# Optimization experiments

Hardware: AMD Instinct MI355X
Metric: run time of the kernel (lower is better)

The kernel has to match this reference:

```python
import jax, jax.numpy as jnp
import numpy as np

H = 1024      # hidden_dim
NH = 16       # num_heads
HD = H // NH  # head_dim
FFN = 4096
EPS = 1e-5


def setup_inputs() -> dict:
    key = jax.random.key(0)
    ks = jax.random.split(key, 12)
    s = 0.02
    return {
        "x": jax.random.normal(ks[0], (2, 2048, H), dtype=jnp.float32),
        "w_qkv": jax.random.normal(ks[1], (H, 3 * H), dtype=jnp.float32) * s,
        "b_qkv": jnp.zeros((3 * H,), dtype=jnp.float32),
        "w_out": jax.random.normal(ks[2], (H, H), dtype=jnp.float32) * s,
        "b_out": jnp.zeros((H,), dtype=jnp.float32),
        "ln1_g": jnp.ones((H,), dtype=jnp.float32),
        "ln1_b": jnp.zeros((H,), dtype=jnp.float32),
        "ln2_g": jnp.ones((H,), dtype=jnp.float32),
        "ln2_b": jnp.zeros((H,), dtype=jnp.float32),
        "w1": jax.random.normal(ks[3], (H, FFN), dtype=jnp.float32) * s,
        "b1": jnp.zeros((FFN,), dtype=jnp.float32),
        "w2": jax.random.normal(ks[4], (FFN, H), dtype=jnp.float32) * s,
        "b2": jnp.zeros((H,), dtype=jnp.float32),
    }


def _layernorm(x, g, b):
    mu = jnp.mean(x, axis=-1, keepdims=True)
    var = jnp.mean(jnp.square(x - mu), axis=-1, keepdims=True)
    return (x - mu) * jax.lax.rsqrt(var + EPS) * g + b


def reference(x, w_qkv, b_qkv, w_out, b_out, ln1_g, ln1_b, ln2_g, ln2_b, w1, b1, w2, b2):
    B, S, _ = x.shape
    # pre-LN attention branch
    h = _layernorm(x, ln1_g, ln1_b)
    qkv = h @ w_qkv + b_qkv                       # (B,S,3H)
    qkv = qkv.reshape(B, S, 3, NH, HD).transpose(2, 0, 3, 1, 4)
    q, k, v = qkv[0], qkv[1], qkv[2]              # (B,NH,S,HD)
    scores = jnp.einsum("bhqd,bhkd->bhqk", q, k) / jnp.sqrt(jnp.float32(HD))
    causal = jnp.triu(jnp.ones((S, S), dtype=bool), k=1)
    scores = jnp.where(causal, -jnp.inf, scores)
    attn = jax.nn.softmax(scores, axis=-1)
    out = jnp.einsum("bhqk,bhkd->bhqd", attn, v)  # (B,NH,S,HD)
    out = out.transpose(0, 2, 1, 3).reshape(B, S, H)
    attn_out = out @ w_out + b_out
    x = x + attn_out
    # FFN branch
    h2 = _layernorm(x, ln2_g, ln2_b)
    ffn = jax.nn.gelu(h2 @ w1 + b1, approximate=False) @ w2 + b2
    return x + ffn
```

## Files before the change

kernel.cpp:

```cpp
#include <hip/hip_runtime.h>
#include <hip/hip_bf16.h>

typedef __bf16 bf16_t;
typedef __bf16 bf16x8 __attribute__((ext_vector_type(8)));
typedef __bf16 bf16x4 __attribute__((ext_vector_type(4)));
typedef __bf16 bf16x2 __attribute__((ext_vector_type(2)));
typedef float  f32x4  __attribute__((ext_vector_type(4)));

#define HDIM 1024
#define SEQ  2048
#define NHEAD 16
#define HEADD 64

__device__ __forceinline__ void gld_lds16(const void* g, void* l) {
  __builtin_amdgcn_global_load_lds(
      (const __attribute__((address_space(1))) unsigned int*)g,
      (__attribute__((address_space(3))) unsigned int*)l, 16, 0, 0);
}

__global__ __launch_bounds__(256) void ln_kernel(const float* __restrict__ x,
                                                 const float* __restrict__ gam,
                                                 const float* __restrict__ bet,
                                                 bf16_t* __restrict__ out) {
  int row = blockIdx.x;
  int t = threadIdx.x;
  const float4* xr = (const float4*)(x + (size_t)row * HDIM);
  float4 v = xr[t];
  float s = v.x + v.y + v.z + v.w;
  float ss = v.x*v.x + v.y*v.y + v.z*v.z + v.w*v.w;
  #pragma unroll
  for (int o = 32; o > 0; o >>= 1) {
    s  += __shfl_xor(s, o);
    ss += __shfl_xor(ss, o);
  }
  __shared__ float red[8];
  int w = t >> 6;
  if ((t & 63) == 0) { red[w*2] = s; red[w*2+1] = ss; }
  __syncthreads();
  s  = red[0] + red[2] + red[4] + red[6];
  ss = red[1] + red[3] + red[5] + red[7];
  float mu  = s * (1.0f / HDIM);
  float var = ss * (1.0f / HDIM) - mu * mu;
  float rstd = rsqrtf(var + 1e-5f);
  float4 g4 = ((const float4*)gam)[t];
  float4 b4 = ((const float4*)bet)[t];
  bf16x4 o4;
  o4[0] = (bf16_t)((v.x - mu) * rstd * g4.x + b4.x);
  o4[1] = (bf16_t)((v.y - mu) * rstd * g4.y + b4.y);
  o4[2] = (bf16_t)((v.z - mu) * rstd * g4.z + b4.z);
  o4[3] = (bf16_t)((v.w - mu) * rstd * g4.w + b4.w);
  *(bf16x4*)(out + (size_t)row * HDIM + t * 4) = o4;
}

__global__ __launch_bounds__(256) void transpose_cast(const float* __restrict__ W,
                                                      bf16_t* __restrict__ Wt,
                                                      int Kd, int Nd) {
  __shared__ float tile[32][33];
  int n0 = blockIdx.x * 32, k0 = blockIdx.y * 32;
  int tx = threadIdx.x & 31, ty = threadIdx.x >> 5;
  #pragma unroll
  for (int i = 0; i < 4; i++)
    tile[ty + i*8][tx] = W[(size_t)(k0 + ty + i*8) * Nd + n0 + tx];
  __syncthreads();
  #pragma unroll
  for (int i = 0; i < 4; i++)
    Wt[(size_t)(n0 + ty + i*8) * Kd + k0 + tx] = (bf16_t)tile[tx][ty + i*8];
}

__device__ __forceinline__ float gelu_fast(float x) {
  float y = 0.7978845608f * (x + 0.044715f * x * x * x);
  float u = exp2f(y * 2.885390082f);
  float th = 1.0f - 2.0f * __builtin_amdgcn_rcpf(u + 1.0f);
  return 0.5f * x * (1.0f + th);
}

template<int EPI, int BN>
__global__ __launch_bounds__(256, 2)
void gemm_bt(const bf16_t* __restrict__ A, const bf16_t* __restrict__ Bt,
             const float* __restrict__ bias, const float* __restrict__ resid,
             void* __restrict__ outp, int M, int N, int K) {
  constexpr int NFRAG = BN / 32;
  __shared__ bf16_t As[2][128*64];
  __shared__ bf16_t Bs[2][BN*64];
  int t = threadIdx.x;
  int w = t >> 6, l = t & 63;
  int wr = w >> 1, wc = w & 1;

  int nbx = gridDim.x;
  int bid = blockIdx.y * nbx + blockIdx.x;
  int chunkx = (nbx * gridDim.y) >> 3;
  int nb = (bid & 7) * chunkx + (bid >> 3);
  int bm = nb / nbx, bn = nb % nbx;
  size_t m0 = (size_t)bm * 128, n0 = (size_t)bn * BN;

  f32x4 acc[4][NFRAG];
  #pragma unroll
  for (int m = 0; m < 4; m++)
    #pragma unroll
    for (int n = 0; n < NFRAG; n++) acc[m][n] = (f32x4)(0.0f);

  int srow = t >> 3;
  int scol = ((t & 7) ^ (srow & 7)) * 8;
  int dsto = t * 8;
  const bf16_t* ag = A  + (m0 + srow) * K + scol;
  const bf16_t* bg = Bt + (n0 + srow) * K + scol;

  int lr = l & 15, lg = l >> 4;

  auto stage = [&](int buf, int k0) {
    #pragma unroll
    for (int p = 0; p < 4; p++)
      gld_lds16(ag + k0 + (size_t)(p*32)*K, &As[buf][dsto + p*32*64]);
    #pragma unroll
    for (int p = 0; p < BN/32; p++)
      gld_lds16(bg + k0 + (size_t)(p*32)*K, &Bs[buf][dsto + p*32*64]);
  };

  stage(0, 0);
  __syncthreads();
  int cur = 0;
  const int NK = K / 64;
  for (int k = 0; k < NK; k++) {
    if (k + 1 < NK) stage(cur ^ 1, (k + 1) * 64);
    #pragma unroll
    for (int kk = 0; kk < 2; kk++) {
      bf16x8 af[4], bfr[NFRAG];
      #pragma unroll
      for (int m = 0; m < 4; m++) {
        int row = wr*64 + m*16 + lr;
        int off = row*128 + (((kk*4 + lg) ^ (row & 7)) << 4);
        af[m] = *(const bf16x8*)((const char*)&As[cur][0] + off);
      }
      #pragma unroll
      for (int n = 0; n < NFRAG; n++) {
        int row = wc*(BN/2) + n*16 + lr;
        int off = row*128 + (((kk*4 + lg) ^ (row & 7)) << 4);
        bfr[n] = *(const bf16x8*)((const char*)&Bs[cur][0] + off);
      }
      #pragma unroll
      for (int m = 0; m < 4; m++)
        #pragma unroll
        for (int n = 0; n < NFRAG; n++)
          acc[m][n] = __builtin_amdgcn_mfma_f32_16x16x32_bf16(af[m], bfr[n], acc[m][n], 0, 0, 0);
    }
    __syncthreads();
    cur ^= 1;
  }

  int r0 = (l >> 4) * 4, c0 = l & 15;
  #pragma unroll
  for (int m = 0; m < 4; m++) {
    #pragma unroll
    for (int n = 0; n < NFRAG; n++) {
      size_t row = m0 + wr*64 + m*16 + r0;
      size_t col = n0 + wc*(BN/2) + n*16 + c0;
      float bv = bias[col];
      #pragma unroll
      for (int r = 0; r < 4; r++) {
        float vv = acc[m][n][r] + bv;
        size_t idx = (row + r) * (size_t)N + col;
        if (EPI == 0) {
          ((bf16_t*)outp)[idx] = (bf16_t)vv;
        } else if (EPI == 1) {
          ((float*)outp)[idx] = vv + resid[idx];
        } else {
          ((bf16_t*)outp)[idx] = (bf16_t)gelu_fast(vv);
        }
      }
    }
  }
}

__global__ __launch_bounds__(512, 4)
void attn_kernel(const bf16_t* __restrict__ qkv, bf16_t* __restrict__ out) {
  int idx = blockIdx.x;
  int half = idx >> 8;
  int sub = idx & 255;
  int qth = sub >> 5;
  int qt = half ? qth : (15 - qth);
  int bh = sub & 31;
  int b = bh >> 4, h = bh & 15;
  int t = threadIdx.x, w = t >> 6, l = t & 63;

  __shared__ bf16_t Ks[2][64*64];
  __shared__ bf16_t Vt[2][64*72];
  __shared__ bf16_t Ps[8][16*64];

  const size_t RS = 3 * HDIM;
  const bf16_t* qb = qkv + (size_t)b * SEQ * RS + h * HEADD;
  const bf16_t* kb = qb + HDIM;
  const bf16_t* vb = qb + 2 * HDIM;

  int lr = l & 15, lg = l >> 4;
  const float SCALE = 0.125f * 1.44269504f;

  bf16x8 qf[2];
  {
    size_t qrow = (size_t)qt * 128 + w * 16 + lr;
    qf[0] = *(const bf16x8*)(qb + qrow * RS + lg * 8);
    qf[1] = *(const bf16x8*)(qb + qrow * RS + 32 + lg * 8);
    #pragma unroll
    for (int i = 0; i < 8; i++) {
      qf[0][i] = (bf16_t)((float)qf[0][i] * SCALE);
      qf[1][i] = (bf16_t)((float)qf[1][i] * SCALE);
    }
  }

  f32x4 o[4];
  #pragma unroll
  for (int d = 0; d < 4; d++) o[d] = (f32x4)(0.0f);
  float m = -1e30f, lsum = 0.0f;

  int srow = t >> 3, scol = (t & 7) * 8;
  int Fv = ((scol >> 3) & 7) << 3;
  int nkt = 2 * qt + 2;

  const bf16_t* kg0 = kb + (size_t)srow * RS + scol;
  const bf16_t* vg0 = vb + (size_t)srow * RS + scol;

  bf16x8 kr = *(const bf16x8*)kg0;
  bf16x8 vr = *(const bf16x8*)vg0;

  int wrow0 = qt * 128 + w * 16;
  int qg = wrow0 + lr;
  bf16_t* pw = Ps[w];
  int psw = (lr & 7) << 4;
  int cur = 0;

  for (int kt = 0; kt < nkt; kt++) {
    {
      int ba = srow * 128 + scol * 2;
      int sw = (srow & 7) << 4;
      *(bf16x8*)((char*)Ks[cur] + (ba ^ sw)) = kr;
      int ksw = srow ^ Fv;
      bf16_t* vt = Vt[cur];
      #pragma unroll
      for (int i = 0; i < 8; i++)
        vt[(scol + i) * 72 + ksw] = vr[i];
    }
    if (kt + 1 < nkt) {
      kr = *(const bf16x8*)(kg0 + (size_t)(kt + 1) * 64 * RS);
      vr = *(const bf16x8*)(vg0 + (size_t)(kt + 1) * 64 * RS);
    }
    __syncthreads();

    bool skipw = (kt * 64) > (wrow0 + 15);
    if (!skipw) {
      f32x4 sc[4];
      #pragma unroll
      for (int kt2 = 0; kt2 < 4; kt2++) {
        sc[kt2] = (f32x4)(0.0f);
        #pragma unroll
        for (int kk = 0; kk < 2; kk++) {
          int row = kt2 * 16 + lr;
          int off = (row * 128 + kk * 64 + lg * 16) ^ ((row & 7) << 4);
          bf16x8 kf = *(const bf16x8*)((char*)Ks[cur] + off);
          sc[kt2] = __builtin_amdgcn_mfma_f32_16x16x32_bf16(kf, qf[kk], sc[kt2], 0, 0, 0);
        }
      }
      if (kt * 64 + 63 > wrow0) {
        #pragma unroll
        for (int kt2 = 0; kt2 < 4; kt2++) {
          #pragma unroll
          for (int r = 0; r < 4; r++) {
            int kcol = kt*64 + kt2*16 + lg*4 + r;
            if (kcol > qg) sc[kt2][r] = -1e30f;
          }
        }
      }
      float tm0 = fmaxf(fmaxf(sc[0][0], sc[0][1]), fmaxf(sc[0][2], sc[0][3]));
      float tm1 = fmaxf(fmaxf(sc[1][0], sc[1][1]), fmaxf(sc[1][2], sc[1][3]));
      float tm2 = fmaxf(fmaxf(sc[2][0], sc[2][1]), fmaxf(sc[2][2], sc[2][3]));
      float tm3 = fmaxf(fmaxf(sc[3][0], sc[3][1]), fmaxf(sc[3][2], sc[3][3]));
      float tm = fmaxf(fmaxf(tm0, tm1), fmaxf(tm2, tm3));
      tm = fmaxf(tm, __shfl_xor(tm, 16));
      tm = fmaxf(tm, __shfl_xor(tm, 32));
      if (!__all(tm <= m + 8.0f)) {
        float nm = fmaxf(m, tm);
        float alpha = exp2f(m - nm);
        m = nm;
        lsum *= alpha;
        #pragma unroll
        for (int d = 0; d < 4; d++)
          #pragma unroll
          for (int r = 0; r < 4; r++) o[d][r] *= alpha;
      }
      #pragma unroll
      for (int kt2 = 0; kt2 < 4; kt2++) {
        float p0 = exp2f(sc[kt2][0] - m);
        float p1 = exp2f(sc[kt2][1] - m);
        float p2 = exp2f(sc[kt2][2] - m);
        float p3 = exp2f(sc[kt2][3] - m);
        lsum += (p0 + p1) + (p2 + p3);
        bf16x2 pa; pa[0] = (bf16_t)p0; pa[1] = (bf16_t)p1;
        bf16x2 pb; pb[0] = (bf16_t)p2; pb[1] = (bf16_t)p3;
        int base = lr * 128 + kt2 * 32 + lg * 8;
        *(bf16x2*)((char*)pw + ((base)     ^ psw)) = pa;
        *(bf16x2*)((char*)pw + ((base + 4) ^ psw)) = pb;
      }
      asm volatile("s_waitcnt lgkmcnt(0)" ::: "memory");
      #pragma unroll
      for (int kk = 0; kk < 2; kk++) {
        int poff = (lr * 128 + kk * 64 + lg * 16) ^ psw;
        bf16x8 pf = *(const bf16x8*)((char*)pw + poff);
        #pragma unroll
        for (int dblk = 0; dblk < 4; dblk++) {
          int vrow = dblk * 16 + lr;
          int Fd = ((vrow >> 3) & 7) << 3;
          bf16x8 vf = *(const bf16x8*)(Vt[cur] + vrow * 72 + ((kk * 32 + lg * 8) ^ Fd));
          o[dblk] = __builtin_amdgcn_mfma_f32_16x16x32_bf16(vf, pf, o[dblk], 0, 0, 0);
        }
      }
    }
    cur ^= 1;
  }

  lsum += __shfl_xor(lsum, 16);
  lsum += __shfl_xor(lsum, 32);
  float inv = 1.0f / lsum;

  bf16_t* ob = out + ((size_t)b * SEQ + qg) * HDIM + h * HEADD;
  #pragma unroll
  for (int dblk = 0; dblk < 4; dblk++) {
    bf16x4 q4;
    #pragma unroll
    for (int r = 0; r < 4; r++) q4[r] = (bf16_t)(o[dblk][r] * inv);
    *(bf16x4*)(ob + dblk * 16 + lg * 4) = q4;
  }
}

extern "C" void kernel_launch(void* const* d_in, const int* in_sizes, int n_in,
                              void* d_out, int out_size, void* d_ws, size_t ws_size,
                              hipStream_t stream) {
  (void)in_sizes; (void)n_in; (void)out_size; (void)ws_size;
  const float* x     = (const float*)d_in[0];
  const float* w_qkv = (const float*)d_in[1];
  const float* b_qkv = (const float*)d_in[2];
  const float* w_out = (const float*)d_in[3];
  const float* b_out = (const float*)d_in[4];
  const float* ln1_g = (const float*)d_in[5];
  const float* ln1_b = (const float*)d_in[6];
  const float* ln2_g = (const float*)d_in[7];
  const float* ln2_b = (const float*)d_in[8];
  const float* w1    = (const float*)d_in[9];
  const float* b1    = (const float*)d_in[10];
  const float* w2    = (const float*)d_in[11];
  const float* b2    = (const float*)d_in[12];
  float* out = (float*)d_out;

  char* ws = (char*)d_ws;
  size_t off = 0;
  auto alloc = [&](size_t bytes) -> void* {
    void* p = ws + off;
    off += (bytes + 255) & ~(size_t)255;
    return p;
  };
  bf16_t* wqkvT = (bf16_t*)alloc((size_t)3072*1024*2);
  bf16_t* woutT = (bf16_t*)alloc((size_t)1024*1024*2);
  bf16_t* w1T   = (bf16_t*)alloc((size_t)4096*1024*2);
  bf16_t* w2T   = (bf16_t*)alloc((size_t)1024*4096*2);
  bf16_t* ln1o  = (bf16_t*)alloc((size_t)4096*1024*2);
  bf16_t* qkvb  = (bf16_t*)alloc((size_t)4096*4096*2);
  bf16_t* attno = (bf16_t*)alloc((size_t)4096*1024*2);
  float*  x2    = (float*) alloc((size_t)4096*1024*4);
  bf16_t* h2 = ln1o;
  bf16_t* g  = qkvb;

  dim3 blk(256);
  transpose_cast<<<dim3(3072/32, 1024/32), blk, 0, stream>>>(w_qkv, wqkvT, 1024, 3072);
  transpose_cast<<<dim3(1024/32, 1024/32), blk, 0, stream>>>(w_out, woutT, 1024, 1024);
  transpose_cast<<<dim3(4096/32, 1024/32), blk, 0, stream>>>(w1,    w1T,   1024, 4096);
  transpose_cast<<<dim3(1024/32, 4096/32), blk, 0, stream>>>(w2,    w2T,   4096, 1024);

  ln_kernel<<<4096, blk, 0, stream>>>(x, ln1_g, ln1_b, ln1o);
  gemm_bt<0,128><<<dim3(24, 32), blk, 0, stream>>>(ln1o, wqkvT, b_qkv, nullptr, qkvb, 4096, 3072, 1024);
  attn_kernel<<<512, dim3(512), 0, stream>>>(qkvb, attno);
  gemm_bt<1,64><<<dim3(16, 32), blk, 0, stream>>>(attno, woutT, b_out, x, x2, 4096, 1024, 1024);
  ln_kernel<<<4096, blk, 0, stream>>>(x2, ln2_g, ln2_b, h2);
  gemm_bt<2,128><<<dim3(32, 32), blk, 0, stream>>>(h2, w1T, b1, nullptr, g, 4096, 4096, 1024);
  gemm_bt<1,64><<<dim3(16, 32), blk, 0, stream>>>(g, w2T, b2, x2, out, 4096, 1024, 4096);
}
```

Before: 237.8 us.

## Split-K the FFN down-projection GEMM with a bf16 partial reduce kernel

Result: faster. 231.2 us (-2.8%).

```diff
diff --git a/kernel.cpp b/kernel.cpp
--- a/kernel.cpp
+++ b/kernel.cpp
@@ -74,7 +74,32 @@
   return 0.5f * x * (1.0f + th);
 }
 
-template<int EPI, int BN>
+__global__ __launch_bounds__(256)
+void reduce2_kernel(const bf16_t* __restrict__ p0, const bf16_t* __restrict__ p1,
+                    const float* __restrict__ bias, const float* __restrict__ resid,
+                    float* __restrict__ out) {
+  size_t base = ((size_t)blockIdx.x * 256 + threadIdx.x) * 8;
+  bf16x8 a = *(const bf16x8*)(p0 + base);
+  bf16x8 b = *(const bf16x8*)(p1 + base);
+  int col = (int)(base & (HDIM - 1));
+  float4 bi0 = *(const float4*)(bias + col);
+  float4 bi1 = *(const float4*)(bias + col + 4);
+  float4 r0 = *(const float4*)(resid + base);
+  float4 r1 = *(const float4*)(resid + base + 4);
+  float4 o0, o1;
+  o0.x = (float)a[0] + (float)b[0] + bi0.x + r0.x;
+  o0.y = (float)a[1] + (float)b[1] + bi0.y + r0.y;
+  o0.z = (float)a[2] + (float)b[2] + bi0.z + r0.z;
+  o0.w = (float)a[3] + (float)b[3] + bi0.w + r0.w;
+  o1.x = (float)a[4] + (float)b[4] + bi1.x + r1.x;
+  o1.y = (float)a[5] + (float)b[5] + bi1.y + r1.y;
+  o1.z = (float)a[6] + (float)b[6] + bi1.z + r1.z;
+  o1.w = (float)a[7] + (float)b[7] + bi1.w + r1.w;
+  *(float4*)(out + base)     = o0;
+  *(float4*)(out + base + 4) = o1;
+}
+
+template<int EPI, int BN, int SPLITK>
 __global__ __launch_bounds__(256, 2)
 void gemm_bt(const bf16_t* __restrict__ A, const bf16_t* __restrict__ Bt,
              const float* __restrict__ bias, const float* __restrict__ resid,
@@ -93,6 +118,9 @@
   int bm = nb / nbx, bn = nb % nbx;
   size_t m0 = (size_t)bm * 128, n0 = (size_t)bn * BN;
 
+  const int KK = (SPLITK > 1) ? K / SPLITK : K;
+  const size_t koff = (SPLITK > 1) ? (size_t)blockIdx.z * KK : 0;
+
   f32x4 acc[4][NFRAG];
   #pragma unroll
   for (int m = 0; m < 4; m++)
@@ -102,8 +130,8 @@
   int srow = t >> 3;
   int scol = ((t & 7) ^ (srow & 7)) * 8;
   int dsto = t * 8;
-  const bf16_t* ag = A  + (m0 + srow) * K + scol;
-  const bf16_t* bg = Bt + (n0 + srow) * K + scol;
+  const bf16_t* ag = A  + (m0 + srow) * K + koff + scol;
+  const bf16_t* bg = Bt + (n0 + srow) * K + koff + scol;
 
   int lr = l & 15, lg = l >> 4;
 
@@ -119,7 +147,7 @@
   stage(0, 0);
   __syncthreads();
   int cur = 0;
-  const int NK = K / 64;
+  const int NK = KK / 64;
   for (int k = 0; k < NK; k++) {
     if (k + 1 < NK) stage(cur ^ 1, (k + 1) * 64);
     #pragma unroll
@@ -148,13 +176,16 @@
   }
 
   int r0 = (l >> 4) * 4, c0 = l & 15;
+  bf16_t* pd = nullptr;
+  if (EPI == 3)
+    pd = (bf16_t*)(blockIdx.z == 0 ? outp : (void*)resid);
   #pragma unroll
   for (int m = 0; m < 4; m++) {
     #pragma unroll
     for (int n = 0; n < NFRAG; n++) {
       size_t row = m0 + wr*64 + m*16 + r0;
       size_t col = n0 + wc*(BN/2) + n*16 + c0;
-      float bv = bias[col];
+      float bv = (EPI == 3) ? 0.0f : bias[col];
       #pragma unroll
       for (int r = 0; r < 4; r++) {
         float vv = acc[m][n][r] + bv;
@@ -163,8 +194,10 @@
           ((bf16_t*)outp)[idx] = (bf16_t)vv;
         } else if (EPI == 1) {
           ((float*)outp)[idx] = vv + resid[idx];
+        } else if (EPI == 2) {
+          ((bf16_t*)outp)[idx] = (bf16_t)gelu_fast(vv);
         } else {
-          ((bf16_t*)outp)[idx] = (bf16_t)gelu_fast(vv);
+          pd[idx] = (bf16_t)vv;
         }
       }
     }
@@ -365,6 +398,8 @@
   float*  x2    = (float*) alloc((size_t)4096*1024*4);
   bf16_t* h2 = ln1o;
   bf16_t* g  = qkvb;
+  bf16_t* part0 = ln1o;
+  bf16_t* part1 = attno;
 
   dim3 blk(256);
   transpose_cast<<<dim3(3072/32, 1024/32), blk, 0, stream>>>(w_qkv, wqkvT, 1024, 3072);
@@ -373,10 +408,11 @@
   transpose_cast<<<dim3(1024/32, 4096/32), blk, 0, stream>>>(w2,    w2T,   4096, 1024);
 
   ln_kernel<<<4096, blk, 0, stream>>>(x, ln1_g, ln1_b, ln1o);
-  gemm_bt<0,128><<<dim3(24, 32), blk, 0, stream>>>(ln1o, wqkvT, b_qkv, nullptr, qkvb, 4096, 3072, 1024);
+  gemm_bt<0,128,1><<<dim3(24, 32), blk, 0, stream>>>(ln1o, wqkvT, b_qkv, nullptr, qkvb, 4096, 3072, 1024);
   attn_kernel<<<512, dim3(512), 0, stream>>>(qkvb, attno);
-  gemm_bt<1,64><<<dim3(16, 32), blk, 0, stream>>>(attno, woutT, b_out, x, x2, 4096, 1024, 1024);
+  gemm_bt<1,64,1><<<dim3(16, 32), blk, 0, stream>>>(attno, woutT, b_out, x, x2, 4096, 1024, 1024);
   ln_kernel<<<4096, blk, 0, stream>>>(x2, ln2_g, ln2_b, h2);
-  gemm_bt<2,128><<<dim3(32, 32), blk, 0, stream>>>(h2, w1T, b1, nullptr, g, 4096, 4096, 1024);
-  gemm_bt<1,64><<<dim3(16, 32), blk, 0, stream>>>(g, w2T, b2, x2, out, 4096, 1024, 4096);
-}
+  gemm_bt<2,128,1><<<dim3(32, 32), blk, 0, stream>>>(h2, w1T, b1, nullptr, g, 4096, 4096, 1024);
+  gemm_bt<3,128,2><<<dim3(8, 32, 2), blk, 0, stream>>>(g, w2T, b2, (const float*)part1, part0, 4096, 1024, 4096);
+  reduce2_kernel<<<2048, blk, 0, stream>>>(part0, part1, b2, x2, out);
+}
```
